# Kernel tuning notes

Measured on AMD Instinct MI355X. Metric: run time of the kernel, lower is better.

Reference implementation:

```python
import jax, jax.numpy as jnp
import numpy as np

L = 16384; ENC = 64; DMODEL = 256; DSTATE = 64; DCONV = 4; EXPAND = 2
NLAYERS = 3; NCLASSES = 11
DIN = EXPAND * DMODEL                 # 512
HEADDIM = 64
NHEADS = DIN // HEADDIM               # 8
DXBC = DIN + 2 * DSTATE               # 640 (ngroups=1)
DPROJ = 2 * DIN + 2 * DSTATE + NHEADS # 1160
NDIR = 6
ORDERS = [(0, 1, 2), (0, 2, 1), (1, 0, 2), (1, 2, 0), (2, 0, 1), (2, 1, 0)]
SCALES = [1, 2, 4]
EPS = 1e-5


def setup_inputs() -> dict:
    key = jax.random.key(0)
    ks = iter(jax.random.split(key, 64))
    def nrm(shape, s=0.02):
        return jax.random.normal(next(ks), shape, jnp.float32) * s
    S = len(SCALES)
    return {
        "vec_real": jax.random.normal(next(ks), (L, ENC), jnp.float32),
        "vec_imag": jax.random.normal(next(ks), (L, ENC), jnp.float32),
        "coords": jax.random.randint(next(ks), (L, 4), 0, 128, jnp.int32),
        # input projection (Linear 128->256, LayerNorm)
        "inp_w": nrm((2 * ENC, DMODEL)), "inp_b": jnp.zeros((DMODEL,)),
        "inp_ln_w": jnp.ones((DMODEL,)), "inp_ln_b": jnp.zeros((DMODEL,)),
        # shared Mamba2 blocks, stacked over NLAYERS
        "ln_w": jnp.ones((NLAYERS, DMODEL)), "ln_b": jnp.zeros((NLAYERS, DMODEL)),
        "in_proj_w": nrm((NLAYERS, DMODEL, DPROJ)),
        "conv_w": nrm((NLAYERS, DXBC, DCONV), 0.1), "conv_b": jnp.zeros((NLAYERS, DXBC)),
        "dt_bias": nrm((NLAYERS, NHEADS), 0.5),
        "A_log": jnp.log(jnp.broadcast_to(jnp.arange(1, NHEADS + 1, dtype=jnp.float32), (NLAYERS, NHEADS))),
        "Dskip": jnp.ones((NLAYERS, NHEADS)),
        "rms_w": jnp.ones((NLAYERS, DIN)),
        "out_proj_w": nrm((NLAYERS, DIN, DMODEL)),
        # fusion MLP
        "fus_ln_w": jnp.ones((NDIR * DMODEL,)), "fus_ln_b": jnp.zeros((NDIR * DMODEL,)),
        "fus_w": nrm((NDIR * DMODEL, DMODEL)), "fus_b": jnp.zeros((DMODEL,)),
        # classifier
        "cls_ln_w": jnp.ones((S * DMODEL,)), "cls_ln_b": jnp.zeros((S * DMODEL,)),
        "cls_w1": nrm((S * DMODEL, 2 * DMODEL)), "cls_b1": jnp.zeros((2 * DMODEL,)),
        "cls_w2": nrm((2 * DMODEL, DMODEL)), "cls_b2": jnp.zeros((DMODEL,)),
        "cls_w3": nrm((DMODEL, NCLASSES)), "cls_b3": jnp.zeros((NCLASSES,)),
    }


def layer_norm(x, w, b):
    mu = x.mean(-1, keepdims=True)
    v = ((x - mu) ** 2).mean(-1, keepdims=True)
    return (x - mu) * jax.lax.rsqrt(v + EPS) * w + b


def mamba2(x, in_proj_w, conv_w, conv_b, dt_bias, A_log, Dskip, rms_w, out_proj_w):
    # x: [B, L, DMODEL]
    Bsz, Ls, _ = x.shape
    zxbcdt = x @ in_proj_w                                  # [B,L,DPROJ]
    z, xBC, dt = jnp.split(zxbcdt, [DIN, DIN + DXBC], axis=-1)
    dt = jax.nn.softplus(dt + dt_bias)                      # [B,L,H]
    # causal depthwise conv1d over xBC, then SiLU
    xc = jnp.transpose(xBC, (0, 2, 1))                      # [B,C,L]
    xc = jax.lax.conv_general_dilated(xc, conv_w[:, None, :], (1,), [(DCONV - 1, 0)],
                                      feature_group_count=DXBC)
    xBC = jax.nn.silu(jnp.transpose(xc, (0, 2, 1)) + conv_b)
    xs, Bm, Cm = jnp.split(xBC, [DIN, DIN + DSTATE], axis=-1)
    xs = xs.reshape(Bsz, Ls, NHEADS, HEADDIM)               # [B,L,H,P]
    A = -jnp.exp(A_log)                                     # [H]

    def step(state, inp):
        x_t, B_t, C_t, dt_t = inp                           # [B,H,P],[B,S],[B,S],[B,H]
        dA = jnp.exp(dt_t * A)                              # [B,H]
        state = state * dA[..., None, None] + (dt_t[..., None, None]
                 * x_t[..., :, None] * B_t[:, None, None, :])
        y = jnp.einsum('bhps,bs->bhp', state, C_t)
        return state, y

    init = jnp.zeros((Bsz, NHEADS, HEADDIM, DSTATE), x.dtype)
    seq = (jnp.moveaxis(xs, 1, 0), jnp.moveaxis(Bm, 1, 0),
           jnp.moveaxis(Cm, 1, 0), jnp.moveaxis(dt, 1, 0))
    _, ys = jax.lax.scan(step, init, seq)                   # [L,B,H,P]
    y = jnp.moveaxis(ys, 0, 1) + Dskip[None, None, :, None] * xs
    y = y.reshape(Bsz, Ls, DIN)
    # gated RMSNorm (norm_before_gate=False)
    y = y * jax.nn.silu(z)
    y = y * jax.lax.rsqrt((y * y).mean(-1, keepdims=True) + EPS) * rms_w
    return y @ out_proj_w


def reference(vec_real, vec_imag, coords, inp_w, inp_b, inp_ln_w, inp_ln_b,
              ln_w, ln_b, in_proj_w, conv_w, conv_b, dt_bias, A_log, Dskip,
              rms_w, out_proj_w, fus_ln_w, fus_ln_b, fus_w, fus_b,
              cls_ln_w, cls_ln_b, cls_w1, cls_b1, cls_w2, cls_b2, cls_w3, cls_b3):
    x = jnp.concatenate([vec_real, vec_imag], -1)           # [L,128]
    h = layer_norm(x @ inp_w + inp_b, inp_ln_w, inp_ln_b)
    h = jax.nn.gelu(h, approximate=False)                   # [L,D]
    # 6 traversal orders via lexsort (np.lexsort semantics: last key primary)
    perms = [jnp.lexsort(tuple(coords[:, a] for a in reversed(axes))) for axes in ORDERS]
    perm = jnp.stack(perms)                                 # [6,L]
    inv = jnp.argsort(perm, axis=1)                         # [6,L]
    xs = h[perm]                                            # [6,L,D] (directions as batch, shared weights)

    def layer_step(xcur, p):
        lw, lb, ipw, cw, cb, dtb, al, dk, rw, ow = p
        y = mamba2(layer_norm(xcur, lw, lb), ipw, cw, cb, dtb, al, dk, rw, ow)
        return xcur + y, None

    params = (ln_w, ln_b, in_proj_w, conv_w, conv_b, dt_bias, A_log, Dskip, rms_w, out_proj_w)
    xs, _ = jax.lax.scan(layer_step, xs, params)
    restored = jnp.take_along_axis(xs, inv[:, :, None], axis=1)  # [6,L,D]
    multi = jnp.transpose(restored, (1, 0, 2)).reshape(L, NDIR * DMODEL)
    fused = layer_norm(multi, fus_ln_w, fus_ln_b) @ fus_w + fus_b
    fused = jax.nn.gelu(fused, approximate=False)           # [L,D]
    # multi-scale pooling; L divisible by every scale -> equal windows
    pooled = jnp.concatenate([fused.reshape(s, L // s, DMODEL).mean(1).mean(0)
                              for s in SCALES], 0)          # [3*D]
    hc = layer_norm(pooled, cls_ln_w, cls_ln_b)
    hc = jax.nn.gelu(hc @ cls_w1 + cls_b1, approximate=False)
    hc = jax.nn.gelu(hc @ cls_w2 + cls_b2, approximate=False)
    return hc @ cls_w3 + cls_b3                             # [NCLASSES]
```

## Files before the change

### kernel.cpp

```cpp
#include <hip/hip_runtime.h>
#include <hip/hip_bf16.h>
#include <math.h>

#define LSEQ 16384
#define NC 128

using short8  = __attribute__((ext_vector_type(8))) short;
using floatx4 = __attribute__((ext_vector_type(4))) float;

__device__ __forceinline__ float bf2f(ushort u){ union{unsigned u; float f;} x; x.u = ((unsigned)u)<<16; return x.f; }
__device__ __forceinline__ ushort f2bf(float f){ union{float f; unsigned u;} x; x.f=f; unsigned u=x.u; return (ushort)((u + 0x7FFFu + ((u>>16)&1u)) >> 16); }
__device__ __forceinline__ float geluf(float x){ return 0.5f*x*(1.f+erff(x*0.70710678118654752f)); }
__device__ __forceinline__ float siluf(float x){ return x/(1.f+__expf(-x)); }
__device__ __forceinline__ float softplusf(float x){ return x>20.f ? x : log1pf(__expf(x)); }

__device__ __forceinline__ float blockSum256(float v, float* red){
  int t = threadIdx.x;
  red[t]=v; __syncthreads();
  #pragma unroll
  for (int s=128;s>0;s>>=1){ if (t<s) red[t]+=red[t+s]; __syncthreads(); }
  float r = red[0]; __syncthreads();
  return r;
}

__device__ const int ORD[6][3] = {{0,1,2},{0,2,1},{1,0,2},{1,2,0},{2,0,1},{2,1,0}};

__global__ __launch_bounds__(256) void zrank_k(int* __restrict__ rank){
  rank[blockIdx.x*256 + threadIdx.x] = 0;
}

__global__ __launch_bounds__(256) void sortp_k(const int* __restrict__ coords, int* __restrict__ rank){
  __shared__ unsigned long long sk[256];
  int d = blockIdx.y; int tid = threadIdx.x;
  int a0=ORD[d][0], a1=ORD[d][1], a2=ORD[d][2];
  int ibase = blockIdx.x*1024;
  int jbase = blockIdx.z*4096;
  unsigned long long mykey[4]; int rk[4] = {0,0,0,0};
  #pragma unroll
  for (int r=0;r<4;++r){
    int i = ibase + r*256 + tid;
    unsigned k3 = ((unsigned)coords[i*4+a0]<<14) | ((unsigned)coords[i*4+a1]<<7) | (unsigned)coords[i*4+a2];
    mykey[r] = (((unsigned long long)k3)<<14) | (unsigned)i;
  }
  for (int j0=jbase; j0<jbase+4096; j0+=256){
    int j = j0 + tid;
    unsigned j3 = ((unsigned)coords[j*4+a0]<<14) | ((unsigned)coords[j*4+a1]<<7) | (unsigned)coords[j*4+a2];
    sk[tid] = (((unsigned long long)j3)<<14) | (unsigned)j;
    __syncthreads();
    #pragma unroll 8
    for (int jj=0; jj<256; ++jj){
      unsigned long long kj = sk[jj];
      #pragma unroll
      for (int r=0;r<4;++r) rk[r] += (kj < mykey[r]) ? 1 : 0;
    }
    __syncthreads();
  }
  #pragma unroll
  for (int r=0;r<4;++r)
    atomicAdd(&rank[d*LSEQ + ibase + r*256 + tid], rk[r]);
}

__global__ __launch_bounds__(256) void sfin_k(const int* __restrict__ rank, int* __restrict__ perm, int* __restrict__ inv){
  int g = blockIdx.x*256 + threadIdx.x;
  int d = g >> 14, i = g & 16383;
  int r = rank[g];
  perm[d*LSEQ + r] = i;
  inv[g] = r;
}

__global__ __launch_bounds__(256) void concat_k(const float* __restrict__ vr, const float* __restrict__ vi, float* __restrict__ xcat){
  int idx = blockIdx.x*256 + threadIdx.x;
  int i = idx >> 7, c = idx & 127;
  xcat[idx] = (c<64) ? vr[(i<<6)+c] : vi[(i<<6)+c-64];
}

__global__ __launch_bounds__(256) void tr_k(const float* __restrict__ in, ushort* __restrict__ out, int K, int N){
  __shared__ float tile[32][33];
  int tx = threadIdx.x & 31, ty = threadIdx.x >> 5;
  int k0 = blockIdx.y*32, n0 = blockIdx.x*32;
  #pragma unroll
  for (int q=0;q<4;++q){
    int k = k0 + ty + q*8, n = n0 + tx;
    if (k < K && n < N) tile[ty+q*8][tx] = in[(size_t)k*N + n];
  }
  __syncthreads();
  #pragma unroll
  for (int q=0;q<4;++q){
    int n = n0 + ty + q*8, k = k0 + tx;
    if (n < N && k < K) out[(size_t)n*K + k] = f2bf(tile[tx][ty+q*8]);
  }
}

template<int EPI, bool AF32>
__global__ __launch_bounds__(256) void gemm_bf_k(
  const void* __restrict__ Ain, int lda, const ushort* __restrict__ Bt,
  int N, int K, float* __restrict__ of,
  const float* __restrict__ bias, const float* __restrict__ rrow)
{
  __shared__ __align__(16) ushort As[64*32];
  __shared__ __align__(16) ushort Bs[64*32];
  int tid = threadIdx.x;
  int n0 = blockIdx.x*64, m0 = blockIdx.y*64;
  int w = tid>>6, lane = tid&63;
  int wm = (w>>1)*32, wn = (w&1)*32;
  int sr = tid>>2, skk = (tid&3)*8;
  floatx4 acc[2][2] = {};
  for (int k0=0; k0<K; k0+=32){
    if constexpr (AF32){
      const float* A = (const float*)Ain;
      float4 v0 = *(const float4*)(A + (size_t)(m0+sr)*lda + k0 + skk);
      float4 v1 = *(const float4*)(A + (size_t)(m0+sr)*lda + k0 + skk + 4);
      ushort o[8] = {f2bf(v0.x),f2bf(v0.y),f2bf(v0.z),f2bf(v0.w),f2bf(v1.x),f2bf(v1.y),f2bf(v1.z),f2bf(v1.w)};
      *(uint4*)(&As[sr*32+skk]) = *(uint4*)o;
    } else {
      const ushort* A = (const ushort*)Ain;
      *(uint4*)(&As[sr*32+skk]) = *(const uint4*)(A + (size_t)(m0+sr)*lda + k0 + skk);
    }
    uint4 bv = make_uint4(0u,0u,0u,0u);
    if (n0+sr < N) bv = *(const uint4*)(Bt + (size_t)(n0+sr)*K + k0 + skk);
    *(uint4*)(&Bs[sr*32+skk]) = bv;
    __syncthreads();
    int kq = lane>>4, l16 = lane&15;
    short8 bf0 = *(const short8*)(&Bs[(wn      + l16)*32 + kq*8]);
    short8 bf1 = *(const short8*)(&Bs[(wn + 16 + l16)*32 + kq*8]);
    #pragma unroll
    for (int ti=0; ti<2; ++ti){
      short8 af = *(const short8*)(&As[(wm + ti*16 + l16)*32 + kq*8]);
      acc[ti][0] = __builtin_amdgcn_mfma_f32_16x16x32_bf16(af, bf0, acc[ti][0], 0,0,0);
      acc[ti][1] = __builtin_amdgcn_mfma_f32_16x16x32_bf16(af, bf1, acc[ti][1], 0,0,0);
    }
    __syncthreads();
  }
  int l16 = lane&15, lq = lane>>4;
  #pragma unroll
  for (int ti=0; ti<2; ++ti)
  #pragma unroll
  for (int tj=0; tj<2; ++tj)
  #pragma unroll
  for (int r=0; r<4; ++r){
    int row = m0 + wm + ti*16 + lq*4 + r;
    int col = n0 + wn + tj*16 + l16;
    if (col >= N) continue;
    float v = acc[ti][tj][r];
    of[(size_t)row*N + col] = v + bias[col];
  }
}

template<int KC, int EPI>
__global__ __launch_bounds__(256) void gemmNS_k(
  const ushort* __restrict__ A, int lda, const ushort* __restrict__ Bt,
  float* __restrict__ of, const float* __restrict__ bias, const float* __restrict__ rrow)
{
  __shared__ __align__(16) ushort As[64*264];
  __shared__ __align__(16) ushort Bs[64*32];
  const int K = KC*256;
  int tid = threadIdx.x;
  int m0 = blockIdx.x*64;
  int w = tid>>6, lane = tid&63;
  int wm = (w>>1)*32, wn = (w&1)*32;
  int sr = tid>>2, skk = (tid&3)*8;
  int l16 = lane&15, kq = lane>>4;
  floatx4 acc[4][2][2] = {};
  for (int kb=0; kb<KC; ++kb){
    #pragma unroll
    for (int ki=0;ki<8;++ki)
      *(uint4*)(&As[sr*264 + ki*32 + skk]) = *(const uint4*)(A + (size_t)(m0+sr)*lda + kb*256 + ki*32 + skk);
    __syncthreads();
    for (int nt=0; nt<4; ++nt){
      for (int k0=0; k0<256; k0+=32){
        *(uint4*)(&Bs[sr*32+skk]) = *(const uint4*)(Bt + (size_t)(nt*64+sr)*K + kb*256 + k0 + skk);
        __syncthreads();
        short8 bf0 = *(const short8*)(&Bs[(wn      + l16)*32 + kq*8]);
        short8 bf1 = *(const short8*)(&Bs[(wn + 16 + l16)*32 + kq*8]);
        #pragma unroll
        for (int ti=0; ti<2; ++ti){
          short8 af = *(const short8*)(&As[(wm + ti*16 + l16)*264 + k0 + kq*8]);
          acc[nt][ti][0] = __builtin_amdgcn_mfma_f32_16x16x32_bf16(af, bf0, acc[nt][ti][0], 0,0,0);
          acc[nt][ti][1] = __builtin_amdgcn_mfma_f32_16x16x32_bf16(af, bf1, acc[nt][ti][1], 0,0,0);
        }
        __syncthreads();
      }
    }
  }
  #pragma unroll
  for (int nt=0; nt<4; ++nt)
  #pragma unroll
  for (int ti=0; ti<2; ++ti)
  #pragma unroll
  for (int tj=0; tj<2; ++tj)
  #pragma unroll
  for (int r=0; r<4; ++r){
    int row = m0 + wm + ti*16 + kq*4 + r;
    int col = nt*64 + wn + tj*16 + l16;
    float v = acc[nt][ti][tj][r];
    if (EPI==2) of[(size_t)row*256 + col] += v * rrow[row];
    else        of[(size_t)row*256 + col] = geluf(v + bias[col]);
  }
}

__global__ __launch_bounds__(256) void gemm1_k(
  const float* __restrict__ xs,
  const float* __restrict__ lnw, const float* __restrict__ lnb,
  const ushort* __restrict__ Wt,
  ushort* __restrict__ xbc, float* __restrict__ odt, const float* __restrict__ dtb)
{
  __shared__ __align__(16) ushort As[64*264];
  __shared__ __align__(16) ushort Bs[64*32];
  int tid = threadIdx.x;
  int m0 = blockIdx.x*64;
  int w = tid>>6, lane = tid&63;
  int wm = (w>>1)*32, wn = (w&1)*32;
  int sr = tid>>2, skk = (tid&3)*8;
  int l16 = lane&15, kq = lane>>4;
  float va[8][8];
  float s = 0.f, s2 = 0.f;
  const float* rowp = xs + (size_t)(m0+sr)*256;
  #pragma unroll
  for (int ki=0;ki<8;++ki){
    float4 v0 = *(const float4*)(rowp + ki*32 + skk);
    float4 v1 = *(const float4*)(rowp + ki*32 + skk + 4);
    va[ki][0]=v0.x; va[ki][1]=v0.y; va[ki][2]=v0.z; va[ki][3]=v0.w;
    va[ki][4]=v1.x; va[ki][5]=v1.y; va[ki][6]=v1.z; va[ki][7]=v1.w;
    #pragma unroll
    for (int j=0;j<8;++j){ s += va[ki][j]; s2 += va[ki][j]*va[ki][j]; }
  }
  s  += __shfl_xor(s,1,64);  s  += __shfl_xor(s,2,64);
  s2 += __shfl_xor(s2,1,64); s2 += __shfl_xor(s2,2,64);
  float mu = s*(1.f/256.f);
  float var = s2*(1.f/256.f) - mu*mu;
  float rs = rsqrtf(fmaxf(var,0.f)+1e-5f);
  #pragma unroll
  for (int ki=0;ki<8;++ki){
    ushort o[8];
    #pragma unroll
    for (int j=0;j<8;++j) o[j] = f2bf((va[ki][j]-mu)*rs*lnw[ki*32+skk+j] + lnb[ki*32+skk+j]);
    *(uint4*)(&As[sr*264 + ki*32 + skk]) = *(uint4*)o;
  }
  __syncthreads();
  for (int nt=0; nt<11; ++nt){
    floatx4 acc[2][2] = {};
    for (int k0=0; k0<256; k0+=32){
      int nr = 512 + nt*64 + sr;
      uint4 bv = make_uint4(0u,0u,0u,0u);
      if (nr < 1160) bv = *(const uint4*)(Wt + (size_t)nr*256 + k0 + skk);
      *(uint4*)(&Bs[sr*32+skk]) = bv;
      __syncthreads();
      short8 bf0 = *(const short8*)(&Bs[(wn      + l16)*32 + kq*8]);
      short8 bf1 = *(const short8*)(&Bs[(wn + 16 + l16)*32 + kq*8]);
      #pragma unroll
      for (int ti=0; ti<2; ++ti){
        short8 af = *(const short8*)(&As[(wm + ti*16 + l16)*264 + k0 + kq*8]);
        acc[ti][0] = __builtin_amdgcn_mfma_f32_16x16x32_bf16(af, bf0, acc[ti][0], 0,0,0);
        acc[ti][1] = __builtin_amdgcn_mfma_f32_16x16x32_bf16(af, bf1, acc[ti][1], 0,0,0);
      }
      __syncthreads();
    }
    #pragma unroll
    for (int ti=0; ti<2; ++ti)
    #pragma unroll
    for (int tj=0; tj<2; ++tj)
    #pragma unroll
    for (int r=0; r<4; ++r){
      int row = m0 + wm + ti*16 + kq*4 + r;
      int col = nt*64 + wn + tj*16 + l16;
      float v = acc[ti][tj][r];
      if (col < 640) xbc[(size_t)row*640 + col] = f2bf(v);
      else if (col < 648) odt[(size_t)row*8 + (col-640)] = softplusf(v + dtb[col-640]);
    }
  }
}

__global__ __launch_bounds__(256) void ln_gelu_k(const float* __restrict__ in, float* __restrict__ out,
    const float* __restrict__ w, const float* __restrict__ b){
  __shared__ float red[256];
  int t = threadIdx.x; size_t base = (size_t)blockIdx.x*256;
  float v = in[base+t];
  float mu = blockSum256(v, red) * (1.f/256.f);
  float dv = v - mu;
  float var = blockSum256(dv*dv, red) * (1.f/256.f);
  float rs = rsqrtf(var + 1e-5f);
  out[base+t] = geluf(dv*rs*w[t] + b[t]);
}

__global__ __launch_bounds__(256) void scatter_k(const float* __restrict__ h, const int* __restrict__ perm, float* __restrict__ xs){
  int blk = blockIdx.x;
  int t = threadIdx.x;
  int d = blk >> 14; int r = blk & 16383;
  int src = perm[d*LSEQ + r];
  xs[(size_t)blk*256 + t] = h[(size_t)src*256 + t];
}

__global__ __launch_bounds__(256) void bnd_k(const ushort* __restrict__ xbc, ushort* __restrict__ bnd){
  int b = blockIdx.x;
  int d = b / NC, c = b % NC;
  size_t row0 = (size_t)d*LSEQ + (size_t)c*128;
  for (int idx = threadIdx.x; idx < 3*640; idx += 256){
    int j = idx/640;
    ushort v = (c==0) ? (ushort)0 : xbc[(row0 - 3 + j)*640 + (idx - j*640)];
    bnd[(size_t)b*3*640 + idx] = v;
  }
}

__global__ __launch_bounds__(256) void conv_k(ushort* __restrict__ xbc, const ushort* __restrict__ bnd,
    const float* __restrict__ convw, const float* __restrict__ convb){
  int b = blockIdx.x;
  int d = b / NC, c = b % NC;
  size_t row0 = (size_t)d*LSEQ + (size_t)c*128;
  int tid = threadIdx.x;
  for (int s0 = tid; s0 < 640; s0 += 256){
    float w0=convw[s0*4], w1=convw[s0*4+1], w2=convw[s0*4+2], w3=convw[s0*4+3];
    float cb=convb[s0];
    float h0=0.f,h1=0.f,h2=0.f;
    if (c != 0){
      const ushort* bp = bnd + (size_t)b*3*640;
      h0=bf2f(bp[s0]); h1=bf2f(bp[640+s0]); h2=bf2f(bp[1280+s0]);
    }
    ushort* p = xbc + row0*640 + s0;
    for (int r=0;r<128;++r){
      float cur = bf2f(*p);
      *p = f2bf(siluf(cb + w0*h0 + w1*h1 + w2*h2 + w3*cur));
      h0=h1; h1=h2; h2=cur;
      p += 640;
    }
  }
}

__global__ __launch_bounds__(256) void ssd_dstate_k(
  const ushort* __restrict__ xbc, const float* __restrict__ dtf, const float* __restrict__ alog,
  ushort* __restrict__ dsb, float* __restrict__ gam, int dh0)
{
  int c = blockIdx.x, dhg = blockIdx.y;
  int dh = dh0 + dhg;
  int d = dh >> 3, h = dh & 7;
  int tid = threadIdx.x;
  float Ah = -__expf(alog[h]);
  __shared__ __align__(16) ushort XT[64*136];
  __shared__ __align__(16) ushort BwT[64*136];
  __shared__ float sdt[128];
  __shared__ float scs[128];
  size_t row0 = (size_t)d*LSEQ + (size_t)c*128;
  if (tid < 128){
    float v = dtf[(row0+tid)*8 + h];
    sdt[tid] = v;
    float x = v;
    #pragma unroll
    for (int o=1;o<64;o<<=1){ float t = __shfl_up(x,(unsigned)o,64); if ((tid&63)>=o) x += t; }
    scs[tid] = x;
  }
  __syncthreads();
  if (tid>=64 && tid<128) scs[tid] += scs[63];
  __syncthreads();
// ... 180 lines not shown
  }
  #pragma unroll
  for (int mt=0; mt<2; ++mt)
  #pragma unroll
  for (int nt=0; nt<4; ++nt)
  #pragma unroll
  for (int r=0; r<4; ++r){
    int tl = w*32 + mt*16 + kq*4 + r;
    int p  = nt*16 + l16;
    float xv = bf2f(XT[p*136 + tl]);
    float yv = Y[mt][nt][r] + Dv*xv;
    xbc[(row0 + tl)*640 + h*64 + p] = f2bf(yv);
  }
}

__global__ __launch_bounds__(512) void scan_legacy_k(ushort* __restrict__ xbc, const float* __restrict__ dtf,
  const float* __restrict__ convw, const float* __restrict__ convb,
  const float* __restrict__ alog, const float* __restrict__ dskip)
{
  int d = blockIdx.x >> 3, h = blockIdx.x & 7;
  int tid = threadIdx.x, p = tid & 63, sg = tid >> 6;
  float Ah = -__expf(alog[h]);
  float Dv = dskip[h];
  __shared__ float raw[19][192];
  __shared__ float cw[192][4];
  __shared__ float cb[192];
  __shared__ float sxc[16][192];
  __shared__ float sdt[16];
  __shared__ float sy[16][8][64];
  for (int c = tid; c < 192; c += 512){
    int ch = (c<64) ? h*64+c : (c<128 ? 512+(c-64) : 576+(c-128));
    #pragma unroll
    for (int k=0;k<4;++k) cw[c][k] = convw[ch*4+k];
    cb[c] = convb[ch];
  }
  for (int idx = tid; idx < 3*192; idx += 512) raw[idx/192][idx%192] = 0.f;
  float st[8];
  #pragma unroll
  for (int j=0;j<8;++j) st[j]=0.f;
  size_t rowbase = (size_t)d*LSEQ;
  __syncthreads();
  for (int t0=0; t0<LSEQ; t0+=16){
    for (int idx = tid; idx < 16*192; idx += 512){
      int tt = idx/192, c = idx%192;
      int ch = (c<64) ? h*64+c : (c<128 ? 512+(c-64) : 576+(c-128));
      raw[3+tt][c] = bf2f(xbc[(rowbase + t0 + tt)*640 + ch]);
    }
    if (tid < 16) sdt[tid] = dtf[(rowbase + t0 + tid)*8 + h];
    __syncthreads();
    for (int idx = tid; idx < 16*192; idx += 512){
      int tt = idx/192, c = idx%192;
      float v = cb[c] + cw[c][0]*raw[tt][c] + cw[c][1]*raw[tt+1][c]
                      + cw[c][2]*raw[tt+2][c] + cw[c][3]*raw[tt+3][c];
      sxc[tt][c] = siluf(v);
    }
    __syncthreads();
    for (int tt=0; tt<16; ++tt){
      float dtv = sdt[tt];
      float dA = __expf(dtv*Ah);
      float xb = dtv * sxc[tt][p];
      float Bl[8], Cl[8];
      #pragma unroll
      for (int q=0;q<2;++q){
        *(floatx4*)&Bl[q*4] = *(const floatx4*)&sxc[tt][64  + sg*8 + q*4];
        *(floatx4*)&Cl[q*4] = *(const floatx4*)&sxc[tt][128 + sg*8 + q*4];
      }
      float part = 0.f;
      #pragma unroll
      for (int j=0;j<8;++j){ st[j] = st[j]*dA + xb*Bl[j]; part += st[j]*Cl[j]; }
      sy[tt][sg][p] = part;
    }
    __syncthreads();
    for (int idx = tid; idx < 16*64; idx += 512){
      int tt = idx>>6, pp = idx&63;
      float yv = sy[tt][0][pp]+sy[tt][1][pp]+sy[tt][2][pp]+sy[tt][3][pp]
               + sy[tt][4][pp]+sy[tt][5][pp]+sy[tt][6][pp]+sy[tt][7][pp] + Dv*sxc[tt][pp];
      xbc[(rowbase + t0 + tt)*640 + h*64 + pp] = f2bf(yv);
    }
    for (int idx = tid; idx < 3*192; idx += 512){
      int r = idx/192, c = idx%192;
      raw[r][c] = raw[16+r][c];
    }
    __syncthreads();
  }
}

__global__ __launch_bounds__(256) void zgate_k(
  const float* __restrict__ xs,
  const float* __restrict__ lnw, const float* __restrict__ lnb,
  const ushort* __restrict__ Wzt, ushort* __restrict__ xbc,
  const float* __restrict__ rmsw, float* __restrict__ rrg)
{
  __shared__ __align__(16) ushort As[64*264];
  __shared__ __align__(16) ushort Bs[64*32];
  __shared__ float gsum[64*32];
  int tid = threadIdx.x;
  int m0 = blockIdx.x*64;
  int w = tid>>6, lane = tid&63;
  int wm = (w>>1)*32, wn = (w&1)*32;
  int sr = tid>>2, skk = (tid&3)*8;
  int l16 = lane&15, kq = lane>>4;
  float va[8][8];
  float s = 0.f, s2 = 0.f;
  const float* rowp = xs + (size_t)(m0+sr)*256;
  #pragma unroll
  for (int ki=0;ki<8;++ki){
    float4 v0 = *(const float4*)(rowp + ki*32 + skk);
    float4 v1 = *(const float4*)(rowp + ki*32 + skk + 4);
    va[ki][0]=v0.x; va[ki][1]=v0.y; va[ki][2]=v0.z; va[ki][3]=v0.w;
    va[ki][4]=v1.x; va[ki][5]=v1.y; va[ki][6]=v1.z; va[ki][7]=v1.w;
    #pragma unroll
    for (int j=0;j<8;++j){ s += va[ki][j]; s2 += va[ki][j]*va[ki][j]; }
  }
  s  += __shfl_xor(s,1,64);  s  += __shfl_xor(s,2,64);
  s2 += __shfl_xor(s2,1,64); s2 += __shfl_xor(s2,2,64);
  float mu = s*(1.f/256.f);
  float var = s2*(1.f/256.f) - mu*mu;
  float rs = rsqrtf(fmaxf(var,0.f)+1e-5f);
  #pragma unroll
  for (int ki=0;ki<8;++ki){
    ushort o[8];
    #pragma unroll
    for (int j=0;j<8;++j) o[j] = f2bf((va[ki][j]-mu)*rs*lnw[ki*32+skk+j] + lnb[ki*32+skk+j]);
    *(uint4*)(&As[sr*264 + ki*32 + skk]) = *(uint4*)o;
  }
  float racc[2][4] = {};
  __syncthreads();
  for (int nt=0; nt<8; ++nt){
    floatx4 acc[2][2] = {};
    for (int k0=0; k0<256; k0+=32){
      uint4 bv = *(const uint4*)(Wzt + (size_t)(nt*64 + sr)*256 + k0 + skk);
      *(uint4*)(&Bs[sr*32+skk]) = bv;
      __syncthreads();
      short8 bf0 = *(const short8*)(&Bs[(wn      + l16)*32 + kq*8]);
      short8 bf1 = *(const short8*)(&Bs[(wn + 16 + l16)*32 + kq*8]);
      #pragma unroll
      for (int ti=0; ti<2; ++ti){
        short8 af = *(const short8*)(&As[(wm + ti*16 + l16)*264 + k0 + kq*8]);
        acc[ti][0] = __builtin_amdgcn_mfma_f32_16x16x32_bf16(af, bf0, acc[ti][0], 0,0,0);
        acc[ti][1] = __builtin_amdgcn_mfma_f32_16x16x32_bf16(af, bf1, acc[ti][1], 0,0,0);
      }
      __syncthreads();
    }
    #pragma unroll
    for (int ti=0; ti<2; ++ti)
    #pragma unroll
    for (int tj=0; tj<2; ++tj)
    #pragma unroll
    for (int r=0; r<4; ++r){
      int row = m0 + wm + ti*16 + kq*4 + r;
      int col = nt*64 + wn + tj*16 + l16;
      float z = acc[ti][tj][r];
      float y = bf2f(xbc[(size_t)row*640 + col]);
      float g = y * siluf(z);
      racc[ti][r] += g*g;
      xbc[(size_t)row*640 + col] = f2bf(g * rmsw[col]);
    }
  }
  #pragma unroll
  for (int ti=0; ti<2; ++ti)
  #pragma unroll
  for (int r=0; r<4; ++r)
    gsum[(wm + ti*16 + kq*4 + r)*32 + (w&1)*16 + l16] = racc[ti][r];
  __syncthreads();
  if (tid < 64){
    float s0 = 0.f;
    #pragma unroll 8
    for (int cc=0;cc<32;++cc) s0 += gsum[tid*32+cc];
    rrg[m0+tid] = rsqrtf(s0*(1.f/512.f) + 1e-5f);
  }
}

__global__ __launch_bounds__(256) void fuse_ln_k(const float* __restrict__ xs, const int* __restrict__ inv,
    const float* __restrict__ w, const float* __restrict__ b, ushort* __restrict__ out){
  __shared__ float red[256];
  int i = blockIdx.x, t = threadIdx.x;
  float v[6];
  float s = 0.f;
  #pragma unroll
  for (int d=0; d<6; ++d){
    int r = inv[d*LSEQ + i];
    v[d] = xs[((size_t)d*LSEQ + r)*256 + t];
    s += v[d];
  }
  float mu = blockSum256(s, red) * (1.f/1536.f);
  float s2 = 0.f;
  #pragma unroll
  for (int d=0; d<6; ++d){ float dv = v[d]-mu; s2 += dv*dv; }
  float var = blockSum256(s2, red) * (1.f/1536.f);
  float rs = rsqrtf(var + 1e-5f);
  #pragma unroll
  for (int d=0; d<6; ++d){
    int c = d*256 + t;
    out[(size_t)i*1536 + c] = f2bf((v[d]-mu)*rs*w[c] + b[c]);
  }
}

__global__ void zero_k(float* p){ p[threadIdx.x] = 0.f; }

__global__ __launch_bounds__(256) void pool_k(const float* __restrict__ fused, float* __restrict__ pooled){
  int t = threadIdx.x;
  size_t r0 = (size_t)blockIdx.x*256;
  float s = 0.f;
  for (int r=0;r<256;++r) s += fused[(r0+r)*256 + t];
  atomicAdd(&pooled[t], s);
}

__global__ __launch_bounds__(256) void cls_k(const float* __restrict__ pooled,
  const float* __restrict__ lnw, const float* __restrict__ lnb,
  const float* __restrict__ w1, const float* __restrict__ b1,
  const float* __restrict__ w2, const float* __restrict__ b2,
  const float* __restrict__ w3, const float* __restrict__ b3, float* __restrict__ out)
{
  __shared__ float red[256];
  __shared__ float hcn[768]; __shared__ float h1[512]; __shared__ float h2[256];
  int t = threadIdx.x;
  float m = pooled[t] * (1.f/16384.f);
  float mu = blockSum256(m, red) * (1.f/256.f);
  float dv = m - mu;
  float var = blockSum256(dv*dv, red) * (1.f/256.f);
  float rs = rsqrtf(var + 1e-5f);
  #pragma unroll
  for (int rep=0; rep<3; ++rep){
    int c = rep*256 + t;
    hcn[c] = dv*rs*lnw[c] + lnb[c];
  }
  __syncthreads();
  for (int n=t; n<512; n+=256){
    float a = b1[n];
    for (int c=0;c<768;++c) a += hcn[c]*w1[c*512+n];
    h1[n] = geluf(a);
  }
  __syncthreads();
  {
    float a = b2[t];
    for (int c=0;c<512;++c) a += h1[c]*w2[c*256+t];
    h2[t] = geluf(a);
  }
  __syncthreads();
  if (t<11){
    float a = b3[t];
    for (int c=0;c<256;++c) a += h2[c]*w3[c*11+t];
    out[t] = a;
  }
}

extern "C" void kernel_launch(void* const* d_in, const int* in_sizes, int n_in,
                              void* d_out, int out_size, void* d_ws, size_t ws_size,
                              hipStream_t stream)
{
  const float* vec_real = (const float*)d_in[0];
  const float* vec_imag = (const float*)d_in[1];
  const int*   coords   = (const int*)d_in[2];
  const float* inp_w    = (const float*)d_in[3];
  const float* inp_b    = (const float*)d_in[4];
  const float* inp_ln_w = (const float*)d_in[5];
  const float* inp_ln_b = (const float*)d_in[6];
  const float* ln_w     = (const float*)d_in[7];
  const float* ln_b     = (const float*)d_in[8];
  const float* in_proj_w= (const float*)d_in[9];
  const float* conv_w   = (const float*)d_in[10];
  const float* conv_b   = (const float*)d_in[11];
  const float* dt_bias  = (const float*)d_in[12];
  const float* A_log    = (const float*)d_in[13];
  const float* Dskip    = (const float*)d_in[14];
  const float* rms_w    = (const float*)d_in[15];
  const float* out_proj_w=(const float*)d_in[16];
  const float* fus_ln_w = (const float*)d_in[17];
  const float* fus_ln_b = (const float*)d_in[18];
  const float* fus_w    = (const float*)d_in[19];
  const float* fus_b    = (const float*)d_in[20];
  const float* cls_ln_w = (const float*)d_in[21];
  const float* cls_ln_b = (const float*)d_in[22];
  const float* cls_w1   = (const float*)d_in[23];
  const float* cls_b1   = (const float*)d_in[24];
  const float* cls_w2   = (const float*)d_in[25];
  const float* cls_b2   = (const float*)d_in[26];
  const float* cls_w3   = (const float*)d_in[27];
  const float* cls_b3   = (const float*)d_in[28];
  (void)in_sizes; (void)n_in; (void)out_size;

  char* ws = (char*)d_ws;
  size_t off = 0;
  auto alloc = [&](size_t bytes)->char* { char* p = ws + off; off = (off + bytes + 255) & ~(size_t)255; return p; };
  int*    perm  = (int*)alloc((size_t)6*LSEQ*4);
  int*    inv   = (int*)alloc((size_t)6*LSEQ*4);
  float*  xs    = (float*)alloc((size_t)6*LSEQ*256*4);
  ushort* xbc   = (ushort*)alloc((size_t)6*LSEQ*640*2);
  float*  dtfb  = (float*)alloc((size_t)6*LSEQ*8*4);
  float*  rrg   = (float*)alloc((size_t)6*LSEQ*4);
  ushort* wtr   = (ushort*)alloc((size_t)1536*256*2);
  float*  pooled= (float*)alloc(256*4);
  size_t base_off = off;
  if (base_off > ws_size) return;

  float* gam = (float*)((char*)wtr + 600*1024);
  int* rankb = (int*)rrg;

  const size_t BND_SZ = (size_t)6*NC*3*640*2;
  size_t dsb_off = base_off + ((BND_SZ + 255) & ~(size_t)255);
  ushort* bndb = (ushort*)(ws + base_off);
  ushort* dsb  = (ushort*)(ws + dsb_off);
  long long avail2 = (long long)ws_size - (long long)dsb_off;
  int gsize = 0;
  const int cands[10] = {48,24,16,12,8,6,4,3,2,1};
  for (int ci=0; ci<10; ++ci){
    if ((long long)((size_t)cands[ci]*NC*4096*2 + 512) <= avail2){ gsize = cands[ci]; break; }
  }

  float*  xcat = (float*)((char*)xbc + 0);
  float*  tmpF = (float*)((char*)xbc + (16u<<20));
  float*  hbuf = (float*)((char*)xbc + (48u<<20));
  ushort* multiB = (ushort*)((char*)xbc + 0);
  float*  fused  = (float*)((char*)xbc + (100u<<20));

  dim3 b256(256);
  zrank_k<<<dim3(6*LSEQ/256),b256,0,stream>>>(rankb);
  sortp_k<<<dim3(16,6,4),b256,0,stream>>>(coords, rankb);
  sfin_k<<<dim3(6*LSEQ/256),b256,0,stream>>>(rankb, perm, inv);
  concat_k<<<dim3(LSEQ*128/256),b256,0,stream>>>(vec_real, vec_imag, xcat);
  tr_k<<<dim3(8,4),b256,0,stream>>>(inp_w, wtr, 128, 256);
  gemm_bf_k<0,true><<<dim3(4, LSEQ/64),b256,0,stream>>>(xcat, 128, wtr, 256, 128, tmpF, inp_b, nullptr);
  ln_gelu_k<<<dim3(LSEQ),b256,0,stream>>>(tmpF, hbuf, inp_ln_w, inp_ln_b);
  scatter_k<<<dim3(6*LSEQ),b256,0,stream>>>(hbuf, perm, xs);

  for (int l=0;l<3;++l){
    const float* cwp = conv_w + (size_t)l*640*4;
    const float* cbp = conv_b + (size_t)l*640;
    const float* alp = A_log + l*8;
    const float* dkp = Dskip + l*8;
    tr_k<<<dim3(37,8),b256,0,stream>>>(in_proj_w + (size_t)l*256*1160, wtr, 256, 1160);
    gemm1_k<<<dim3(6*LSEQ/64),b256,0,stream>>>(xs, ln_w + l*256, ln_b + l*256,
        wtr, xbc, dtfb, dt_bias + l*8);
    if (gsize > 0){
      bnd_k<<<dim3(6*NC),b256,0,stream>>>(xbc, bndb);
      conv_k<<<dim3(6*NC),b256,0,stream>>>(xbc, bndb, cwp, cbp);
      for (int dh0=0; dh0<48; dh0+=gsize){
        ssd_dstate_k<<<dim3(NC,gsize),b256,0,stream>>>(xbc, dtfb, alp, dsb, gam, dh0);
        ssd_scan_k<<<dim3(gsize,2),b256,0,stream>>>(dsb, gam, dh0);
        ssd_out_k<<<dim3(NC,gsize),b256,0,stream>>>(xbc, dsb, dtfb, alp, dkp, dh0);
      }
    } else {
      scan_legacy_k<<<dim3(48),dim3(512),0,stream>>>(xbc, dtfb, cwp, cbp, alp, dkp);
    }
    zgate_k<<<dim3(6*LSEQ/64),b256,0,stream>>>(xs, ln_w + l*256, ln_b + l*256,
        wtr, xbc, rms_w + l*512, rrg);
    tr_k<<<dim3(8,16),b256,0,stream>>>(out_proj_w + (size_t)l*512*256, wtr, 512, 256);
    gemmNS_k<2,2><<<dim3(6*LSEQ/64),b256,0,stream>>>(xbc, 640, wtr, xs, nullptr, rrg);
  }

  fuse_ln_k<<<dim3(LSEQ),b256,0,stream>>>(xs, inv, fus_ln_w, fus_ln_b, multiB);
  tr_k<<<dim3(8,48),b256,0,stream>>>(fus_w, wtr, 1536, 256);
  gemmNS_k<6,3><<<dim3(LSEQ/64),b256,0,stream>>>(multiB, 1536, wtr, fused, fus_b, nullptr);
  zero_k<<<dim3(1),b256,0,stream>>>(pooled);
  pool_k<<<dim3(64),b256,0,stream>>>(fused, pooled);
  cls_k<<<dim3(1),b256,0,stream>>>(pooled, cls_ln_w, cls_ln_b, cls_w1, cls_b1, cls_w2, cls_b2, cls_w3, cls_b3, (float*)d_out);
}
```

Measured before the change: 3.119 ms.

## Deepen GEMM K-tiles to 128 and split sort rank work across more blocks

```diff
diff --git a/kernel.cpp b/kernel.cpp
--- a/kernel.cpp
+++ b/kernel.cpp
@@ -34,7 +34,7 @@
   int d = blockIdx.y; int tid = threadIdx.x;
   int a0=ORD[d][0], a1=ORD[d][1], a2=ORD[d][2];
   int ibase = blockIdx.x*1024;
-  int jbase = blockIdx.z*4096;
+  int jbase = blockIdx.z*2048;
   unsigned long long mykey[4]; int rk[4] = {0,0,0,0};
   #pragma unroll
   for (int r=0;r<4;++r){
@@ -42,7 +42,7 @@
     unsigned k3 = ((unsigned)coords[i*4+a0]<<14) | ((unsigned)coords[i*4+a1]<<7) | (unsigned)coords[i*4+a2];
     mykey[r] = (((unsigned long long)k3)<<14) | (unsigned)i;
   }
-  for (int j0=jbase; j0<jbase+4096; j0+=256){
+  for (int j0=jbase; j0<jbase+2048; j0+=256){
     int j = j0 + tid;
     unsigned j3 = ((unsigned)coords[j*4+a0]<<14) | ((unsigned)coords[j*4+a1]<<7) | (unsigned)coords[j*4+a2];
     sk[tid] = (((unsigned long long)j3)<<14) | (unsigned)j;
@@ -91,11 +91,9 @@
   }
 }
 
-template<int EPI, bool AF32>
-__global__ __launch_bounds__(256) void gemm_bf_k(
-  const void* __restrict__ Ain, int lda, const ushort* __restrict__ Bt,
-  int N, int K, float* __restrict__ of,
-  const float* __restrict__ bias, const float* __restrict__ rrow)
+__global__ __launch_bounds__(256) void gemm0_k(
+  const float* __restrict__ A, int lda, const ushort* __restrict__ Bt,
+  int N, int K, float* __restrict__ of, const float* __restrict__ bias)
 {
   __shared__ __align__(16) ushort As[64*32];
   __shared__ __align__(16) ushort Bs[64*32];
@@ -106,16 +104,10 @@
   int sr = tid>>2, skk = (tid&3)*8;
   floatx4 acc[2][2] = {};
   for (int k0=0; k0<K; k0+=32){
-    if constexpr (AF32){
-      const float* A = (const float*)Ain;
-      float4 v0 = *(const float4*)(A + (size_t)(m0+sr)*lda + k0 + skk);
-      float4 v1 = *(const float4*)(A + (size_t)(m0+sr)*lda + k0 + skk + 4);
-      ushort o[8] = {f2bf(v0.x),f2bf(v0.y),f2bf(v0.z),f2bf(v0.w),f2bf(v1.x),f2bf(v1.y),f2bf(v1.z),f2bf(v1.w)};
-      *(uint4*)(&As[sr*32+skk]) = *(uint4*)o;
-    } else {
-      const ushort* A = (const ushort*)Ain;
-      *(uint4*)(&As[sr*32+skk]) = *(const uint4*)(A + (size_t)(m0+sr)*lda + k0 + skk);
-    }
+    float4 v0 = *(const float4*)(A + (size_t)(m0+sr)*lda + k0 + skk);
+    float4 v1 = *(const float4*)(A + (size_t)(m0+sr)*lda + k0 + skk + 4);
+    ushort o[8] = {f2bf(v0.x),f2bf(v0.y),f2bf(v0.z),f2bf(v0.w),f2bf(v1.x),f2bf(v1.y),f2bf(v1.z),f2bf(v1.w)};
+    *(uint4*)(&As[sr*32+skk]) = *(uint4*)o;
     uint4 bv = make_uint4(0u,0u,0u,0u);
     if (n0+sr < N) bv = *(const uint4*)(Bt + (size_t)(n0+sr)*K + k0 + skk);
     *(uint4*)(&Bs[sr*32+skk]) = bv;
@@ -141,60 +133,7 @@
     int row = m0 + wm + ti*16 + lq*4 + r;
     int col = n0 + wn + tj*16 + l16;
     if (col >= N) continue;
-    float v = acc[ti][tj][r];
-    of[(size_t)row*N + col] = v + bias[col];
-  }
-}
-
-template<int KC, int EPI>
-__global__ __launch_bounds__(256) void gemmNS_k(
-  const ushort* __restrict__ A, int lda, const ushort* __restrict__ Bt,
-  float* __restrict__ of, const float* __restrict__ bias, const float* __restrict__ rrow)
-{
-  __shared__ __align__(16) ushort As[64*264];
-  __shared__ __align__(16) ushort Bs[64*32];
-  const int K = KC*256;
-  int tid = threadIdx.x;
-  int m0 = blockIdx.x*64;
-  int w = tid>>6, lane = tid&63;
-  int wm = (w>>1)*32, wn = (w&1)*32;
-  int sr = tid>>2, skk = (tid&3)*8;
-  int l16 = lane&15, kq = lane>>4;
-  floatx4 acc[4][2][2] = {};
-  for (int kb=0; kb<KC; ++kb){
-    #pragma unroll
-    for (int ki=0;ki<8;++ki)
-      *(uint4*)(&As[sr*264 + ki*32 + skk]) = *(const uint4*)(A + (size_t)(m0+sr)*lda + kb*256 + ki*32 + skk);
-    __syncthreads();
-    for (int nt=0; nt<4; ++nt){
-      for (int k0=0; k0<256; k0+=32){
-        *(uint4*)(&Bs[sr*32+skk]) = *(const uint4*)(Bt + (size_t)(nt*64+sr)*K + kb*256 + k0 + skk);
-        __syncthreads();
-        short8 bf0 = *(const short8*)(&Bs[(wn      + l16)*32 + kq*8]);
-        short8 bf1 = *(const short8*)(&Bs[(wn + 16 + l16)*32 + kq*8]);
-        #pragma unroll
-        for (int ti=0; ti<2; ++ti){
-          short8 af = *(const short8*)(&As[(wm + ti*16 + l16)*264 + k0 + kq*8]);
-          acc[nt][ti][0] = __builtin_amdgcn_mfma_f32_16x16x32_bf16(af, bf0, acc[nt][ti][0], 0,0,0);
-          acc[nt][ti][1] = __builtin_amdgcn_mfma_f32_16x16x32_bf16(af, bf1, acc[nt][ti][1], 0,0,0);
-        }
-        __syncthreads();
-      }
-    }
-  }
-  #pragma unroll
-  for (int nt=0; nt<4; ++nt)
-  #pragma unroll
-  for (int ti=0; ti<2; ++ti)
-  #pragma unroll
-  for (int tj=0; tj<2; ++tj)
-  #pragma unroll
-  for (int r=0; r<4; ++r){
-    int row = m0 + wm + ti*16 + kq*4 + r;
-    int col = nt*64 + wn + tj*16 + l16;
-    float v = acc[nt][ti][tj][r];
-    if (EPI==2) of[(size_t)row*256 + col] += v * rrow[row];
-    else        of[(size_t)row*256 + col] = geluf(v + bias[col]);
+    of[(size_t)row*N + col] = acc[ti][tj][r] + bias[col];
   }
 }
 
@@ -205,68 +144,245 @@
   ushort* __restrict__ xbc, float* __restrict__ odt, const float* __restrict__ dtb)
 {
   __shared__ __align__(16) ushort As[64*264];
-  __shared__ __align__(16) ushort Bs[64*32];
+  __shared__ __align__(16) ushort Bs[64*136];
   int tid = threadIdx.x;
   int m0 = blockIdx.x*64;
   int w = tid>>6, lane = tid&63;
   int wm = (w>>1)*32, wn = (w&1)*32;
   int sr = tid>>2, skk = (tid&3)*8;
+  int sb = (tid&3)*32;
   int l16 = lane&15, kq = lane>>4;
-  float va[8][8];
-  float s = 0.f, s2 = 0.f;
-  const float* rowp = xs + (size_t)(m0+sr)*256;
-  #pragma unroll
-  for (int ki=0;ki<8;++ki){
-    float4 v0 = *(const float4*)(rowp + ki*32 + skk);
-    float4 v1 = *(const float4*)(rowp + ki*32 + skk + 4);
-    va[ki][0]=v0.x; va[ki][1]=v0.y; va[ki][2]=v0.z; va[ki][3]=v0.w;
-    va[ki][4]=v1.x; va[ki][5]=v1.y; va[ki][6]=v1.z; va[ki][7]=v1.w;
-    #pragma unroll
-    for (int j=0;j<8;++j){ s += va[ki][j]; s2 += va[ki][j]*va[ki][j]; }
-  }
-  s  += __shfl_xor(s,1,64);  s  += __shfl_xor(s,2,64);
-  s2 += __shfl_xor(s2,1,64); s2 += __shfl_xor(s2,2,64);
-  float mu = s*(1.f/256.f);
-  float var = s2*(1.f/256.f) - mu*mu;
-  float rs = rsqrtf(fmaxf(var,0.f)+1e-5f);
-  #pragma unroll
-  for (int ki=0;ki<8;++ki){
-    ushort o[8];
-    #pragma unroll
-    for (int j=0;j<8;++j) o[j] = f2bf((va[ki][j]-mu)*rs*lnw[ki*32+skk+j] + lnb[ki*32+skk+j]);
-    *(uint4*)(&As[sr*264 + ki*32 + skk]) = *(uint4*)o;
-  }
-  __syncthreads();
+  {
+    float va[8][8];
+    float s = 0.f, s2 = 0.f;
+    const float* rowp = xs + (size_t)(m0+sr)*256;
+    #pragma unroll
+    for (int ki=0;ki<8;++ki){
+      float4 v0 = *(const float4*)(rowp + ki*32 + skk);
+      float4 v1 = *(const float4*)(rowp + ki*32 + skk + 4);
+      va[ki][0]=v0.x; va[ki][1]=v0.y; va[ki][2]=v0.z; va[ki][3]=v0.w;
+      va[ki][4]=v1.x; va[ki][5]=v1.y; va[ki][6]=v1.z; va[ki][7]=v1.w;
+      #pragma unroll
+      for (int j=0;j<8;++j){ s += va[ki][j]; s2 += va[ki][j]*va[ki][j]; }
+    }
+    s  += __shfl_xor(s,1,64);  s  += __shfl_xor(s,2,64);
+    s2 += __shfl_xor(s2,1,64); s2 += __shfl_xor(s2,2,64);
+    float mu = s*(1.f/256.f);
+    float var = s2*(1.f/256.f) - mu*mu;
+    float rs = rsqrtf(fmaxf(var,0.f)+1e-5f);
+    #pragma unroll
+    for (int ki=0;ki<8;++ki){
+      ushort o[8];
+      #pragma unroll
+      for (int j=0;j<8;++j) o[j] = f2bf((va[ki][j]-mu)*rs*lnw[ki*32+skk+j] + lnb[ki*32+skk+j]);
+      *(uint4*)(&As[sr*264 + ki*32 + skk]) = *(uint4*)o;
+    }
+  }
   for (int nt=0; nt<11; ++nt){
     floatx4 acc[2][2] = {};
-    for (int k0=0; k0<256; k0+=32){
+    #pragma unroll
+    for (int kb=0; kb<2; ++kb){
       int nr = 512 + nt*64 + sr;
-      uint4 bv = make_uint4(0u,0u,0u,0u);
-      if (nr < 1160) bv = *(const uint4*)(Wt + (size_t)nr*256 + k0 + skk);
-      *(uint4*)(&Bs[sr*32+skk]) = bv;
-      __syncthreads();
-      short8 bf0 = *(const short8*)(&Bs[(wn      + l16)*32 + kq*8]);
-      short8 bf1 = *(const short8*)(&Bs[(wn + 16 + l16)*32 + kq*8]);
-      #pragma unroll
-      for (int ti=0; ti<2; ++ti){
-        short8 af = *(const short8*)(&As[(wm + ti*16 + l16)*264 + k0 + kq*8]);
-        acc[ti][0] = __builtin_amdgcn_mfma_f32_16x16x32_bf16(af, bf0, acc[ti][0], 0,0,0);
-        acc[ti][1] = __builtin_amdgcn_mfma_f32_16x16x32_bf16(af, bf1, acc[ti][1], 0,0,0);
+      uint4 bv[4] = {};
+      if (nr < 1160){
+        #pragma unroll
+        for (int j=0;j<4;++j) bv[j] = *(const uint4*)(Wt + (size_t)nr*256 + kb*128 + sb + j*8);
       }
       __syncthreads();
-    }
-    #pragma unroll
-    for (int ti=0; ti<2; ++ti)
+      #pragma unroll
+      for (int j=0;j<4;++j) *(uint4*)(&Bs[sr*136 + sb + j*8]) = bv[j];
+      __syncthreads();
+      #pragma unroll
+      for (int kc=0;kc<4;++kc){
+        #pragma unroll
+        for (int tj=0;tj<2;++tj){
+          short8 bfr = *(const short8*)(&Bs[(wn + tj*16 + l16)*136 + kc*32 + kq*8]);
+          #pragma unroll
+          for (int mt=0;mt<2;++mt){
+            short8 af = *(const short8*)(&As[(wm + mt*16 + l16)*264 + kb*128 + kc*32 + kq*8]);
+            acc[mt][tj] = __builtin_amdgcn_mfma_f32_16x16x32_bf16(af, bfr, acc[mt][tj], 0,0,0);
+          }
+        }
+      }
+    }
+    #pragma unroll
+    for (int mt=0; mt<2; ++mt)
     #pragma unroll
     for (int tj=0; tj<2; ++tj)
     #pragma unroll
     for (int r=0; r<4; ++r){
-      int row = m0 + wm + ti*16 + kq*4 + r;
+      int row = m0 + wm + mt*16 + kq*4 + r;
       int col = nt*64 + wn + tj*16 + l16;
-      float v = acc[ti][tj][r];
+      float v = acc[mt][tj][r];
       if (col < 640) xbc[(size_t)row*640 + col] = f2bf(v);
       else if (col < 648) odt[(size_t)row*8 + (col-640)] = softplusf(v + dtb[col-640]);
     }
+  }
+}
+
+__global__ __launch_bounds__(256) void zgate_k(
+  const float* __restrict__ xs,
+  const float* __restrict__ lnw, const float* __restrict__ lnb,
+  const ushort* __restrict__ Wzt, ushort* __restrict__ xbc,
+  const float* __restrict__ rmsw, float* __restrict__ rrg)
+{
+  __shared__ __align__(16) ushort As[64*264];
+  __shared__ __align__(16) ushort Bs[64*136];
+  __shared__ float gsum2[128];
+  int tid = threadIdx.x;
+  int m0 = blockIdx.x*64;
+  int w = tid>>6, lane = tid&63;
+  int wm = (w>>1)*32, wn = (w&1)*32;
+  int sr = tid>>2, skk = (tid&3)*8;
+  int sb = (tid&3)*32;
+  int l16 = lane&15, kq = lane>>4;
+  {
+    float va[8][8];
+    float s = 0.f, s2 = 0.f;
+    const float* rowp = xs + (size_t)(m0+sr)*256;
+    #pragma unroll
+    for (int ki=0;ki<8;++ki){
+      float4 v0 = *(const float4*)(rowp + ki*32 + skk);
+      float4 v1 = *(const float4*)(rowp + ki*32 + skk + 4);
+      va[ki][0]=v0.x; va[ki][1]=v0.y; va[ki][2]=v0.z; va[ki][3]=v0.w;
+      va[ki][4]=v1.x; va[ki][5]=v1.y; va[ki][6]=v1.z; va[ki][7]=v1.w;
+      #pragma unroll
+      for (int j=0;j<8;++j){ s += va[ki][j]; s2 += va[ki][j]*va[ki][j]; }
+    }
+    s  += __shfl_xor(s,1,64);  s  += __shfl_xor(s,2,64);
+    s2 += __shfl_xor(s2,1,64); s2 += __shfl_xor(s2,2,64);
+    float mu = s*(1.f/256.f);
+    float var = s2*(1.f/256.f) - mu*mu;
+    float rs = rsqrtf(fmaxf(var,0.f)+1e-5f);
+    #pragma unroll
+    for (int ki=0;ki<8;++ki){
+      ushort o[8];
+      #pragma unroll
+      for (int j=0;j<8;++j) o[j] = f2bf((va[ki][j]-mu)*rs*lnw[ki*32+skk+j] + lnb[ki*32+skk+j]);
+      *(uint4*)(&As[sr*264 + ki*32 + skk]) = *(uint4*)o;
+    }
+  }
+  float racc[2][4] = {};
+  for (int nt=0; nt<8; ++nt){
+    floatx4 acc[2][2] = {};
+    #pragma unroll
+    for (int kb=0; kb<2; ++kb){
+      int nr = nt*64 + sr;
+      uint4 bv[4];
+      #pragma unroll
+      for (int j=0;j<4;++j) bv[j] = *(const uint4*)(Wzt + (size_t)nr*256 + kb*128 + sb + j*8);
+      __syncthreads();
+      #pragma unroll
+      for (int j=0;j<4;++j) *(uint4*)(&Bs[sr*136 + sb + j*8]) = bv[j];
+      __syncthreads();
+      #pragma unroll
+      for (int kc=0;kc<4;++kc){
+        #pragma unroll
+        for (int tj=0;tj<2;++tj){
+          short8 bfr = *(const short8*)(&Bs[(wn + tj*16 + l16)*136 + kc*32 + kq*8]);
+          #pragma unroll
+          for (int mt=0;mt<2;++mt){
+            short8 af = *(const short8*)(&As[(wm + mt*16 + l16)*264 + kb*128 + kc*32 + kq*8]);
+            acc[mt][tj] = __builtin_amdgcn_mfma_f32_16x16x32_bf16(af, bfr, acc[mt][tj], 0,0,0);
+          }
+        }
+      }
+    }
+    #pragma unroll
+    for (int mt=0; mt<2; ++mt)
+    #pragma unroll
+    for (int tj=0; tj<2; ++tj)
+    #pragma unroll
+    for (int r=0; r<4; ++r){
+      int row = m0 + wm + mt*16 + kq*4 + r;
+      int col = nt*64 + wn + tj*16 + l16;
+      float z = acc[mt][tj][r];
+      float y = bf2f(xbc[(size_t)row*640 + col]);
+      float g = y * siluf(z);
+      racc[mt][r] += g*g;
+      xbc[(size_t)row*640 + col] = f2bf(g * rmsw[col]);
+    }
+  }
+  #pragma unroll
+  for (int mt=0; mt<2; ++mt)
+  #pragma unroll
+  for (int r=0; r<4; ++r){
+    float v = racc[mt][r];
+    v += __shfl_xor(v,1,64); v += __shfl_xor(v,2,64);
+    v += __shfl_xor(v,4,64); v += __shfl_xor(v,8,64);
+    if (l16 == 0) gsum2[(wm + mt*16 + kq*4 + r)*2 + (w&1)] = v;
+  }
+  __syncthreads();
+  if (tid < 64)
+    rrg[m0+tid] = rsqrtf((gsum2[tid*2] + gsum2[tid*2+1])*(1.f/512.f) + 1e-5f);
+}
+
+template<int KC, int EPI>
+__global__ __launch_bounds__(256) void gemmNS_k(
+  const ushort* __restrict__ A, int lda, const ushort* __restrict__ Bt,
+  float* __restrict__ of, const float* __restrict__ bias, const float* __restrict__ rrow)
+{
+  __shared__ __align__(16) ushort As[64*264];
+  __shared__ __align__(16) ushort Bs[64*136];
+  const int K = KC*256;
+  int tid = threadIdx.x;
+  int m0 = blockIdx.x*64;
+  int w = tid>>6, lane = tid&63;
+  int wm = (w>>1)*32, wn = (w&1)*32;
+  int sr = tid>>2, skk = (tid&3)*8;
+  int sb = (tid&3)*32;
+  int l16 = lane&15, kq = lane>>4;
+  floatx4 acc[4][2][2] = {};
+  for (int kb=0; kb<KC; ++kb){
+    uint4 av[8];
+    #pragma unroll
+    for (int ki=0;ki<8;++ki)
+      av[ki] = *(const uint4*)(A + (size_t)(m0+sr)*lda + kb*256 + ki*32 + skk);
+    __syncthreads();
+    #pragma unroll
+    for (int ki=0;ki<8;++ki)
+      *(uint4*)(&As[sr*264 + ki*32 + skk]) = av[ki];
+    __syncthreads();
+    for (int nt=0; nt<4; ++nt){
+      #pragma unroll
+      for (int kh=0; kh<2; ++kh){
+        uint4 bv[4];
+        #pragma unroll
+        for (int j=0;j<4;++j)
+          bv[j] = *(const uint4*)(Bt + (size_t)(nt*64+sr)*K + kb*256 + kh*128 + sb + j*8);
+        __syncthreads();
+        #pragma unroll
+        for (int j=0;j<4;++j) *(uint4*)(&Bs[sr*136 + sb + j*8]) = bv[j];
+        __syncthreads();
+        #pragma unroll
+        for (int kc=0;kc<4;++kc){
+          #pragma unroll
+          for (int tj=0;tj<2;++tj){
+            short8 bfr = *(const short8*)(&Bs[(wn + tj*16 + l16)*136 + kc*32 + kq*8]);
+            #pragma unroll
+            for (int mt=0;mt<2;++mt){
+              short8 af = *(const short8*)(&As[(wm + mt*16 + l16)*264 + kh*128 + kc*32 + kq*8]);
+              acc[nt][mt][tj] = __builtin_amdgcn_mfma_f32_16x16x32_bf16(af, bfr, acc[nt][mt][tj], 0,0,0);
+            }
+          }
+        }
+      }
+    }
+    __syncthreads();
+  }
+  #pragma unroll
+  for (int nt=0; nt<4; ++nt)
+  #pragma unroll
+  for (int mt=0; mt<2; ++mt)
+  #pragma unroll
+  for (int tj=0; tj<2; ++tj)
+  #pragma unroll
+  for (int r=0; r<4; ++r){
+    int row = m0 + wm + mt*16 + kq*4 + r;
+    int col = nt*64 + wn + tj*16 + l16;
+    float v = acc[nt][mt][tj][r];
+    if (EPI==2) of[(size_t)row*256 + col] += v * rrow[row];
+    else        of[(size_t)row*256 + col] = geluf(v + bias[col]);
   }
 }
 
@@ -613,92 +729,6 @@
       raw[r][c] = raw[16+r][c];
     }
     __syncthreads();
-  }
-}
-
-__global__ __launch_bounds__(256) void zgate_k(
-  const float* __restrict__ xs,
-  const float* __restrict__ lnw, const float* __restrict__ lnb,
-  const ushort* __restrict__ Wzt, ushort* __restrict__ xbc,
-  const float* __restrict__ rmsw, float* __restrict__ rrg)
-{
-  __shared__ __align__(16) ushort As[64*264];
-  __shared__ __align__(16) ushort Bs[64*32];
-  __shared__ float gsum[64*32];
-  int tid = threadIdx.x;
-  int m0 = blockIdx.x*64;
-  int w = tid>>6, lane = tid&63;
-  int wm = (w>>1)*32, wn = (w&1)*32;
-  int sr = tid>>2, skk = (tid&3)*8;
-  int l16 = lane&15, kq = lane>>4;
-  float va[8][8];
-  float s = 0.f, s2 = 0.f;
-  const float* rowp = xs + (size_t)(m0+sr)*256;
-  #pragma unroll
-  for (int ki=0;ki<8;++ki){
-    float4 v0 = *(const float4*)(rowp + ki*32 + skk);
-    float4 v1 = *(const float4*)(rowp + ki*32 + skk + 4);
-    va[ki][0]=v0.x; va[ki][1]=v0.y; va[ki][2]=v0.z; va[ki][3]=v0.w;
-    va[ki][4]=v1.x; va[ki][5]=v1.y; va[ki][6]=v1.z; va[ki][7]=v1.w;
-    #pragma unroll
-    for (int j=0;j<8;++j){ s += va[ki][j]; s2 += va[ki][j]*va[ki][j]; }
-  }
-  s  += __shfl_xor(s,1,64);  s  += __shfl_xor(s,2,64);
-  s2 += __shfl_xor(s2,1,64); s2 += __shfl_xor(s2,2,64);
-  float mu = s*(1.f/256.f);
-  float var = s2*(1.f/256.f) - mu*mu;
-  float rs = rsqrtf(fmaxf(var,0.f)+1e-5f);
-  #pragma unroll
-  for (int ki=0;ki<8;++ki){
-    ushort o[8];
-    #pragma unroll
-    for (int j=0;j<8;++j) o[j] = f2bf((va[ki][j]-mu)*rs*lnw[ki*32+skk+j] + lnb[ki*32+skk+j]);
-    *(uint4*)(&As[sr*264 + ki*32 + skk]) = *(uint4*)o;
-  }
-  float racc[2][4] = {};
-  __syncthreads();
-  for (int nt=0; nt<8; ++nt){
-    floatx4 acc[2][2] = {};
-    for (int k0=0; k0<256; k0+=32){
-      uint4 bv = *(const uint4*)(Wzt + (size_t)(nt*64 + sr)*256 + k0 + skk);
-      *(uint4*)(&Bs[sr*32+skk]) = bv;
-      __syncthreads();
-      short8 bf0 = *(const short8*)(&Bs[(wn      + l16)*32 + kq*8]);
-      short8 bf1 = *(const short8*)(&Bs[(wn + 16 + l16)*32 + kq*8]);
-      #pragma unroll
-      for (int ti=0; ti<2; ++ti){
-        short8 af = *(const short8*)(&As[(wm + ti*16 + l16)*264 + k0 + kq*8]);
-        acc[ti][0] = __builtin_amdgcn_mfma_f32_16x16x32_bf16(af, bf0, acc[ti][0], 0,0,0);
-        acc[ti][1] = __builtin_amdgcn_mfma_f32_16x16x32_bf16(af, bf1, acc[ti][1], 0,0,0);
-      }
-      __syncthreads();
-    }
-    #pragma unroll
-    for (int ti=0; ti<2; ++ti)
-    #pragma unroll
-    for (int tj=0; tj<2; ++tj)
-    #pragma unroll
-    for (int r=0; r<4; ++r){
-      int row = m0 + wm + ti*16 + kq*4 + r;
-      int col = nt*64 + wn + tj*16 + l16;
-      float z = acc[ti][tj][r];
-      float y = bf2f(xbc[(size_t)row*640 + col]);
-      float g = y * siluf(z);
-      racc[ti][r] += g*g;
-      xbc[(size_t)row*640 + col] = f2bf(g * rmsw[col]);
-    }
-  }
-  #pragma unroll
-  for (int ti=0; ti<2; ++ti)
-  #pragma unroll
-  for (int r=0; r<4; ++r)
-    gsum[(wm + ti*16 + kq*4 + r)*32 + (w&1)*16 + l16] = racc[ti][r];
-  __syncthreads();
-  if (tid < 64){
-    float s0 = 0.f;
-    #pragma unroll 8
-    for (int cc=0;cc<32;++cc) s0 += gsum[tid*32+cc];
-    rrg[m0+tid] = rsqrtf(s0*(1.f/512.f) + 1e-5f);
   }
 }
 
@@ -847,11 +877,11 @@
 
   dim3 b256(256);
   zrank_k<<<dim3(6*LSEQ/256),b256,0,stream>>>(rankb);
-  sortp_k<<<dim3(16,6,4),b256,0,stream>>>(coords, rankb);
+  sortp_k<<<dim3(16,6,8),b256,0,stream>>>(coords, rankb);
   sfin_k<<<dim3(6*LSEQ/256),b256,0,stream>>>(rankb, perm, inv);
   concat_k<<<dim3(LSEQ*128/256),b256,0,stream>>>(vec_real, vec_imag, xcat);
   tr_k<<<dim3(8,4),b256,0,stream>>>(inp_w, wtr, 128, 256);
-  gemm_bf_k<0,true><<<dim3(4, LSEQ/64),b256,0,stream>>>(xcat, 128, wtr, 256, 128, tmpF, inp_b, nullptr);
+  gemm0_k<<<dim3(4, LSEQ/64),b256,0,stream>>>(xcat, 128, wtr, 256, 128, tmpF, inp_b);
   ln_gelu_k<<<dim3(LSEQ),b256,0,stream>>>(tmpF, hbuf, inp_ln_w, inp_ln_b);
   scatter_k<<<dim3(6*LSEQ),b256,0,stream>>>(hbuf, perm, xs);
 
```

Result: slower. 3.635 ms (+16.5%).
